# Kernel tuning notes

Hardware: AMD Instinct MI355X
Metric: run time of the kernel (lower is better)

## Reference

```python
import jax, jax.numpy as jnp
import numpy as np


def setup_inputs() -> dict:
    key = jax.random.key(0)
    k1, k2 = jax.random.split(key)
    G, T, H, E = 2, 4096, 2048, 64
    return {
        "token_inputs": jax.random.normal(k1, (G, T, H), dtype=jnp.float32),
        "kernel": jax.random.normal(k2, (H, E), dtype=jnp.float32) * 0.02,
        "bias": jnp.zeros((E,), dtype=jnp.float32),
        "num_experts": E,
        "expert_capacity": 128,
        "num_selected_experts": 2,
    }


def reference(token_inputs, kernel, bias, num_experts, expert_capacity,
              num_selected_experts):
    """TokensChooseMaskedRouter forward (jitter disabled).

    Returns (dispatch_mask, combine_array, auxiliary_loss, router_z_loss).
    """
    x = token_inputs.astype(jnp.float32)
    G, T, _ = x.shape
    E = num_experts
    K = num_selected_experts

    # Router logits + probabilities.
    router_logits = jnp.einsum('gth,he->gte', x, kernel) + bias  # [G,T,E]
    router_probs = jax.nn.softmax(router_logits, axis=-1)

    # Top-k experts per token.
    expert_gate, expert_index = jax.lax.top_k(router_probs, K)  # [G,T,K]

    # Load balancing auxiliary loss (Switch Transformer eq. 4-6).
    expert_mask = jnp.max(jax.nn.one_hot(expert_index, E, dtype=jnp.int32),
                          axis=-2)  # [G,T,E]
    tokens_per_ge = jnp.mean(expert_mask.astype(jnp.float32), axis=-2)
    probs_per_ge = jnp.mean(router_probs, axis=-2, dtype=jnp.float32)
    aux_loss = jnp.mean(tokens_per_ge * probs_per_ge) * (E ** 2)

    # Batch prioritized routing: order tokens by top-1 gate value.
    permutation = jnp.argsort(-expert_gate[..., 0], axis=-1)  # [G,T]
    expert_index = jnp.take_along_axis(expert_index, permutation[..., None],
                                       axis=1)

    # Make selected-expert axis leading, flatten to [G, K*T].
    flat_index = jnp.swapaxes(expert_index, 1, 2).reshape(G, K * T)
    flat_mask = jax.nn.one_hot(flat_index, E, dtype=jnp.int32)  # [G,K*T,E]

    # Position of each token within its chosen expert's buffer.
    token_priority = jnp.cumsum(flat_mask, axis=1) * flat_mask - 1  # [G,K*T,E]
    token_priority = token_priority.reshape(G, K, T, E)
    token_priority = jnp.max(jnp.swapaxes(token_priority, 1, 2), axis=2)  # [G,T,E]

    # Undo the priority permutation.
    inv_permutation = jnp.argsort(permutation, axis=-1)
    token_priority = jnp.take_along_axis(token_priority,
                                         inv_permutation[..., None], axis=1)

    # Tokens with priority >= expert_capacity (or -1) are dropped: one_hot of
    # out-of-range index is all zeros.
    dispatch_mask = jax.nn.one_hot(token_priority, expert_capacity,
                                   dtype=jnp.bool_)  # [G,T,E,C]
    combine_array = router_probs[..., None] * dispatch_mask.astype(jnp.float32)

    # Router z-loss.
    log_z = jax.nn.logsumexp(router_logits, axis=-1)
    z_loss = jnp.sum(log_z ** 2, dtype=jnp.float32) / (G * T)

    return dispatch_mask, combine_array, aux_loss, z_loss
```

## Files before the change

kernel.cpp:

```cpp
#include <hip/hip_runtime.h>
#include <cstdint>
#include <cstddef>

static constexpr int Gn = 2;
static constexpr int Tn = 4096;
static constexpr int Hn = 2048;
static constexpr int En = 64;
static constexpr int CAPn = 128;
static constexpr size_t GT = (size_t)Gn * Tn;
static constexpr size_t GTEC = GT * En * CAPn;
static constexpr size_t GTEC4 = GTEC / 4;

typedef float  f4v __attribute__((ext_vector_type(4)));
typedef double d4v __attribute__((ext_vector_type(4)));

__device__ inline double wave_softmax_topk(
    double logit, int g, int t,
    double* __restrict__ dkey, double* __restrict__ dlogz2,
    int* __restrict__ idx0, int* __restrict__ idx1,
    float* __restrict__ g0f, float* __restrict__ g1f)
{
  const int e = threadIdx.x & 63;
  double m = logit;
  #pragma unroll
  for (int off = 32; off; off >>= 1) {
    double o = __shfl_xor(m, off);
    m = o > m ? o : m;
  }
  double ex = exp(logit - m);
  double s = ex;
  #pragma unroll
  for (int off = 32; off; off >>= 1) s += __shfl_xor(s, off);
  double p = ex / s;
  size_t gt = (size_t)g * Tn + t;

  double bp = p; int bi = e;
  #pragma unroll
  for (int off = 32; off; off >>= 1) {
    double op = __shfl_xor(bp, off);
    int    oi = __shfl_xor(bi, off);
    if (op > bp || (op == bp && oi < bi)) { bp = op; bi = oi; }
  }
  double q = (e == bi) ? -1.0 : p;
  double bp2 = q; int bi2 = e;
  #pragma unroll
  for (int off = 32; off; off >>= 1) {
    double op = __shfl_xor(bp2, off);
    int    oi = __shfl_xor(bi2, off);
    if (op > bp2 || (op == bp2 && oi < bi2)) { bp2 = op; bi2 = oi; }
  }
  if (e == 0) {
    dkey[gt] = bp;
    double lz = m + log(s);
    dlogz2[gt] = lz * lz;
    idx0[gt] = bi;  idx1[gt] = bi2;
    g0f[gt] = (float)bp;  g1f[gt] = (float)bp2;
  }
  return p;
}

__global__ __launch_bounds__(64) void k0_probe(
    double* __restrict__ rowmap, double* __restrict__ colmap)
{
  const int lane = threadIdx.x & 63;
  const double ai = (double)(lane & 15);
  d4v accR = {0., 0., 0., 0.};
  d4v accC = {0., 0., 0., 0.};
  accR = __builtin_amdgcn_mfma_f64_16x16x4f64(ai, 1.0, accR, 0, 0, 0);
  accC = __builtin_amdgcn_mfma_f64_16x16x4f64(1.0, ai, accC, 0, 0, 0);
  #pragma unroll
  for (int r = 0; r < 4; ++r) {
    rowmap[lane * 4 + r] = accR[r];
    colmap[lane * 4 + r] = accC[r];
  }
}

__global__ __launch_bounds__(256, 2) void k1_gemm(
    const float* __restrict__ X, const float* __restrict__ W,
    const float* __restrict__ Bv,
    const double* __restrict__ rowmap, const double* __restrict__ colmap,
    double* __restrict__ dkey, double* __restrict__ dlogz2,
    int* __restrict__ idx0, int* __restrict__ idx1,
    float* __restrict__ g0f, float* __restrict__ g1f,
    double* __restrict__ partial, float* __restrict__ out)
{
  __shared__ double lred[4][16][64];
  __shared__ double pred[4][64];
  const int tid  = threadIdx.x;
  const int lane = tid & 63;
  const int w    = tid >> 6;
  const int bid  = blockIdx.x;
  const int g    = bid >> 8;
  const int tb   = (bid & 255) * 16;
  const size_t gt0 = (size_t)g * Tn + tb;

  const int tl = lane & 15;
  const int kl = lane >> 4;

  int rowm[4], colm[4];
  #pragma unroll
  for (int r = 0; r < 4; ++r) {
    rowm[r] = (int)(rowmap[lane * 4 + r] * 0.25 + 0.5);
    colm[r] = (int)(colmap[lane * 4 + r] * 0.25 + 0.5);
  }

  const float* __restrict__ xa = X + (gt0 + tl) * Hn + w * 512 + kl;
  const float* __restrict__ wb = W + (size_t)(w * 512 + kl) * En + tl;

  f4v* __restrict__ ob = (f4v*)out;
  const f4v zf = {0.f, 0.f, 0.f, 0.f};

  d4v acc0 = {0., 0., 0., 0.};
  d4v acc1 = {0., 0., 0., 0.};
  d4v acc2 = {0., 0., 0., 0.};
  d4v acc3 = {0., 0., 0., 0.};

  for (int k4 = 0; k4 < 128; ++k4) {
    {
      int n1 = k4 * 512 + tid;
      int n2 = n1 + 256;
      size_t i1 = (size_t)(n1 >> 15) * GTEC4 + gt0 * 2048 + (n1 & 32767);
      size_t i2 = (size_t)(n2 >> 15) * GTEC4 + gt0 * 2048 + (n2 & 32767);
      __builtin_nontemporal_store(zf, &ob[i1]);
      __builtin_nontemporal_store(zf, &ob[i2]);
    }
    double a = (double)xa[4 * k4];
    const float* wr = wb + (size_t)(4 * k4) * En;
    double b0 = (double)wr[0];
    double b1 = (double)wr[16];
    double b2 = (double)wr[32];
    double b3 = (double)wr[48];
    acc0 = __builtin_amdgcn_mfma_f64_16x16x4f64(a, b0, acc0, 0, 0, 0);
    acc1 = __builtin_amdgcn_mfma_f64_16x16x4f64(a, b1, acc1, 0, 0, 0);
    acc2 = __builtin_amdgcn_mfma_f64_16x16x4f64(a, b2, acc2, 0, 0, 0);
    acc3 = __builtin_amdgcn_mfma_f64_16x16x4f64(a, b3, acc3, 0, 0, 0);
  }

  #pragma unroll
  for (int r = 0; r < 4; ++r) {
    lred[w][rowm[r]][colm[r]]      = acc0[r];
    lred[w][rowm[r]][16 + colm[r]] = acc1[r];
    lred[w][rowm[r]][32 + colm[r]] = acc2[r];
    lred[w][rowm[r]][48 + colm[r]] = acc3[r];
  }
  __syncthreads();

  const double bv = (double)Bv[lane];
  double psum = 0.0;
  #pragma unroll
  for (int j = 0; j < 4; ++j) {
    int t = w * 4 + j;
    double full = lred[0][t][lane] + lred[1][t][lane]
                + lred[2][t][lane] + lred[3][t][lane] + bv;
    psum += wave_softmax_topk(full, g, tb + t,
                              dkey, dlogz2, idx0, idx1, g0f, g1f);
  }
  pred[w][lane] = psum;
  __syncthreads();
  if (tid < 64) {
    partial[(size_t)bid * 64 + tid] =
        pred[0][tid] + pred[1][tid] + pred[2][tid] + pred[3][tid];
  }
}

__global__ __launch_bounds__(256) void k2_rank(
    const double* __restrict__ dkey,
    const int* __restrict__ idx0, const int* __restrict__ idx1,
    int* __restrict__ perm, int* __restrict__ sidx0, int* __restrict__ sidx1)
{
  __shared__ __align__(16) double keys[Tn];
  __shared__ int rk[32][8];
  const int tid = threadIdx.x;
  const int bid = blockIdx.x;
  const int g    = bid >> 7;
  const int part = bid & 127;
  const size_t gbase = (size_t)g * Tn;
  for (int i = tid; i < Tn; i += 256) keys[i] = dkey[gbase + i];
  __syncthreads();

  const int tl = tid >> 3;
  const int q  = tid & 7;
  const int tg = part * 32 + tl;
  const double k = keys[tg];
  int r = 0;
  #pragma unroll 4
  for (int j2 = q * 512; j2 < q * 512 + 512; j2 += 2) {
    double2 kj = *(const double2*)&keys[j2];
    r += (kj.x > k) || (kj.x == k && (j2     < tg));
    r += (kj.y > k) || (kj.y == k && (j2 + 1 < tg));
  }
  rk[tl][q] = r;
  __syncthreads();
  if (tid < 32) {
    const int tg2 = part * 32 + tid;
    int rr = 0;
    #pragma unroll
    for (int u = 0; u < 8; ++u) rr += rk[tid][u];
    perm[gbase + rr]  = tg2;
    sidx0[gbase + rr] = idx0[gbase + tg2];
    sidx1[gbase + rr] = idx1[gbase + tg2];
  }
}

__global__ __launch_bounds__(256) void k3_prio(
    const int* __restrict__ sidx0, const int* __restrict__ sidx1,
    const int* __restrict__ perm,
    int* __restrict__ prio0, int* __restrict__ prio1, int* __restrict__ cntge)
{
  __shared__ int sc[256];
  const int tid = threadIdx.x;
  const int g = blockIdx.x >> 6;
  const int e = blockIdx.x & 63;
  const size_t gbase = (size_t)g * Tn;
  const int p0 = tid * 16;

  int base = 0;
  #pragma unroll
  for (int ph = 0; ph < 2; ++ph) {
    const int* __restrict__ sidx = ph ? sidx1 : sidx0;
    int* __restrict__ prio = ph ? prio1 : prio0;

    int loc[16];
    const int4* s4 = (const int4*)(sidx + gbase + p0);
    #pragma unroll
    for (int u = 0; u < 4; ++u) {
      int4 v = s4[u];
      loc[u * 4 + 0] = v.x; loc[u * 4 + 1] = v.y;
      loc[u * 4 + 2] = v.z; loc[u * 4 + 3] = v.w;
    }
    int cntl = 0;
    #pragma unroll
    for (int k = 0; k < 16; ++k) cntl += (loc[k] == e);

    __syncthreads();
    sc[tid] = cntl;
    __syncthreads();
    #pragma unroll
    for (int off = 1; off < 256; off <<= 1) {
      int v = (tid >= off) ? sc[tid - off] : 0;
      __syncthreads();
      sc[tid] += v;
      __syncthreads();
    }
    int pr = base + sc[tid] - cntl;
    int total = sc[255];
    #pragma unroll
    for (int k = 0; k < 16; ++k) {
      if (loc[k] == e) {
        prio[gbase + perm[gbase + p0 + k]] = pr;
        ++pr;
      }
    }
    base += total;
  }
  if (tid == 0) cntge[g * En + e] = base;
}

__global__ __launch_bounds__(256) void k5a(
    const double* __restrict__ dlogz2, const double* __restrict__ partial,
    const int* __restrict__ cntge, double* __restrict__ gpart)
{
  __shared__ double red[256];
  const int g = blockIdx.x;
  const int tid = threadIdx.x;

  double z = 0.0;
  for (int i = tid; i < Tn; i += 256) z += dlogz2[(size_t)g * Tn + i];
  red[tid] = z; __syncthreads();
  for (int s = 128; s; s >>= 1) { if (tid < s) red[tid] += red[tid + s]; __syncthreads(); }
  if (tid == 0) gpart[g * 2 + 0] = red[0];
  __syncthreads();

  const int q = tid >> 6, e = tid & 63;
  double s = 0.0;
  for (int i = 0; i < 64; ++i) {
    int b = g * 256 + i * 4 + q;
    s += partial[(size_t)b * 64 + e];
  }
  red[tid] = s; __syncthreads();
  if (tid < 64) {
    double sp = red[tid] + red[64 + tid] + red[128 + tid] + red[192 + tid];
    red[tid] = sp * (double)cntge[g * En + tid];
  }
  __syncthreads();
  for (int st = 32; st; st >>= 1) { if (tid < st) red[tid] += red[tid + st]; __syncthreads(); }
  if (tid == 0) gpart[g * 2 + 1] = red[0];
}

__global__ __launch_bounds__(256) void k6_fill(
    const int* __restrict__ idx0, const int* __restrict__ idx1,
    const int* __restrict__ prio0, const int* __restrict__ prio1,
    const float* __restrict__ g0f, const float* __restrict__ g1f,
    const double* __restrict__ gpart,
    float* __restrict__ out)
{
  const int t = blockIdx.x * 256 + threadIdx.x;
  if (t < (int)GT) {
    const size_t gt = (size_t)t;
    const int e0 = idx0[gt], e1 = idx1[gt];
    const int p0 = prio0[gt], p1 = prio1[gt];
    const size_t slab = gt * (size_t)(En * CAPn);
    if (p0 < CAPn) {
      size_t n = slab + e0 * CAPn + p0;
      out[n] = 1.0f;
      out[GTEC + n] = g0f[gt];
    }
    if (p1 < CAPn) {
      size_t n = slab + e1 * CAPn + p1;
      out[n] = 1.0f;
      out[GTEC + n] = g1f[gt];
    }
  }
  if (t == 0) {
    double aux = (gpart[1] + gpart[3]) * (double)En /
                 ((double)Gn * (double)Tn * (double)Tn);
    double z   = (gpart[0] + gpart[2]) / (double)GT;
    out[GTEC * 2]     = (float)aux;
    out[GTEC * 2 + 1] = (float)z;
  }
}

extern "C" void kernel_launch(void* const* d_in, const int* in_sizes, int n_in,
                              void* d_out, int out_size, void* d_ws, size_t ws_size,
                              hipStream_t stream)
{
  (void)in_sizes; (void)n_in; (void)out_size; (void)ws_size;
  const float* X  = (const float*)d_in[0];
  const float* W  = (const float*)d_in[1];
  const float* Bv = (const float*)d_in[2];
  float* out = (float*)d_out;

  char* ws = (char*)d_ws;
  size_t off = 0;
  auto carve = [&](size_t bytes) -> void* {
    void* p = ws + off;
    off += (bytes + 255) & ~(size_t)255;
    return p;
  };
  double* rowmap  = (double*)carve(64 * 4 * 8);
  double* colmap  = (double*)carve(64 * 4 * 8);
  double* dkey    = (double*)carve(GT * 8);
  double* dlogz2  = (double*)carve(GT * 8);
  double* partial = (double*)carve((size_t)512 * 64 * 8);
  double* gpart   = (double*)carve(4 * 8);
  int* idx0  = (int*)carve(GT * 4);
  int* idx1  = (int*)carve(GT * 4);
  float* g0f = (float*)carve(GT * 4);
  float* g1f = (float*)carve(GT * 4);
  int* perm  = (int*)carve(GT * 4);
  int* sidx0 = (int*)carve(GT * 4);
  int* sidx1 = (int*)carve(GT * 4);
  int* prio0 = (int*)carve(GT * 4);
  int* prio1 = (int*)carve(GT * 4);
  int* cntge = (int*)carve((size_t)Gn * En * 4);

  k0_probe<<<1, 64, 0, stream>>>(rowmap, colmap);
  k1_gemm<<<512, 256, 0, stream>>>(X, W, Bv, rowmap, colmap, dkey, dlogz2,
                                   idx0, idx1, g0f, g1f, partial, out);
  k2_rank<<<Gn * 128, 256, 0, stream>>>(dkey, idx0, idx1, perm, sidx0, sidx1);
  k3_prio<<<Gn * En, 256, 0, stream>>>(sidx0, sidx1, perm, prio0, prio1, cntge);
  k5a<<<Gn, 256, 0, stream>>>(dlogz2, partial, cntge, gpart);
  k6_fill<<<(int)(GT / 256), 256, 0, stream>>>(idx0, idx1, prio0, prio1,
                                               g0f, g1f, gpart, out);
}
```

Baseline: 162.0 us.

## Split zero-fill into dedicated warps and prefetch GEMM operands in k1

Doubles the k1 block to 512 threads: four extra wavefronts do only the nontemporal zero-fill of the output region while the original four wavefronts run the f64 MFMA GEMM, with the next iteration's X and W values loaded a step ahead. The aim is to overlap the large memory-bound zero-store with the compute and load latency of the GEMM instead of interleaving them in one instruction stream. The fill wavefronts call __syncthreads twice before returning to match the barriers in the compute path, which is fragile if that barrier count differs. Higher occupancy bounds may also constrain register allocation.

```diff
diff --git a/kernel.cpp b/kernel.cpp
--- a/kernel.cpp
+++ b/kernel.cpp
@@ -75,7 +75,7 @@
   }
 }
 
-__global__ __launch_bounds__(256, 2) void k1_gemm(
+__global__ __launch_bounds__(512, 4) void k1_gemm(
     const float* __restrict__ X, const float* __restrict__ W,
     const float* __restrict__ Bv,
     const double* __restrict__ rowmap, const double* __restrict__ colmap,
@@ -94,6 +94,21 @@
   const int tb   = (bid & 255) * 16;
   const size_t gt0 = (size_t)g * Tn + tb;
 
+  if (w >= 4) {
+    const int fl = (w - 4) * 64 + lane;
+    f4v* __restrict__ ob = (f4v*)out;
+    const f4v zf = {0.f, 0.f, 0.f, 0.f};
+    #pragma unroll 4
+    for (int it = 0; it < 256; ++it) {
+      int n = it * 256 + fl;
+      size_t i1 = (size_t)(n >> 15) * GTEC4 + gt0 * 2048 + (n & 32767);
+      __builtin_nontemporal_store(zf, &ob[i1]);
+    }
+    __syncthreads();
+    __syncthreads();
+    return;
+  }
+
   const int tl = lane & 15;
   const int kl = lane >> 4;
 
@@ -106,30 +121,27 @@
 
   const float* __restrict__ xa = X + (gt0 + tl) * Hn + w * 512 + kl;
   const float* __restrict__ wb = W + (size_t)(w * 512 + kl) * En + tl;
-
-  f4v* __restrict__ ob = (f4v*)out;
-  const f4v zf = {0.f, 0.f, 0.f, 0.f};
 
   d4v acc0 = {0., 0., 0., 0.};
   d4v acc1 = {0., 0., 0., 0.};
   d4v acc2 = {0., 0., 0., 0.};
   d4v acc3 = {0., 0., 0., 0.};
 
+  float a_n = xa[0];
+  const float* wr0 = wb;
+  float w0_n = wr0[0], w1_n = wr0[16], w2_n = wr0[32], w3_n = wr0[48];
+
   for (int k4 = 0; k4 < 128; ++k4) {
-    {
-      int n1 = k4 * 512 + tid;
-      int n2 = n1 + 256;
-      size_t i1 = (size_t)(n1 >> 15) * GTEC4 + gt0 * 2048 + (n1 & 32767);
-      size_t i2 = (size_t)(n2 >> 15) * GTEC4 + gt0 * 2048 + (n2 & 32767);
-      __builtin_nontemporal_store(zf, &ob[i1]);
-      __builtin_nontemporal_store(zf, &ob[i2]);
-    }
-    double a = (double)xa[4 * k4];
-    const float* wr = wb + (size_t)(4 * k4) * En;
-    double b0 = (double)wr[0];
-    double b1 = (double)wr[16];
-    double b2 = (double)wr[32];
-    double b3 = (double)wr[48];
+    double a  = (double)a_n;
+    double b0 = (double)w0_n;
+    double b1 = (double)w1_n;
+    double b2 = (double)w2_n;
+    double b3 = (double)w3_n;
+    if (k4 < 127) {
+      a_n = xa[4 * (k4 + 1)];
+      const float* wr = wb + (size_t)(4 * (k4 + 1)) * En;
+      w0_n = wr[0]; w1_n = wr[16]; w2_n = wr[32]; w3_n = wr[48];
+    }
     acc0 = __builtin_amdgcn_mfma_f64_16x16x4f64(a, b0, acc0, 0, 0, 0);
     acc1 = __builtin_amdgcn_mfma_f64_16x16x4f64(a, b1, acc1, 0, 0, 0);
     acc2 = __builtin_amdgcn_mfma_f64_16x16x4f64(a, b2, acc2, 0, 0, 0);
@@ -355,7 +367,7 @@
   int* cntge = (int*)carve((size_t)Gn * En * 4);
 
   k0_probe<<<1, 64, 0, stream>>>(rowmap, colmap);
-  k1_gemm<<<512, 256, 0, stream>>>(X, W, Bv, rowmap, colmap, dkey, dlogz2,
+  k1_gemm<<<512, 512, 0, stream>>>(X, W, Bv, rowmap, colmap, dkey, dlogz2,
                                    idx0, idx1, g0f, g1f, partial, out);
   k2_rank<<<Gn * 128, 256, 0, stream>>>(dkey, idx0, idx1, perm, sidx0, sidx1);
   k3_prio<<<Gn * En, 256, 0, stream>>>(sidx0, sidx1, perm, prio0, prio1, cntge);
```

Measured after the change: 175.4 us. +8.3%, slower.
